# Optimization experiments

Hardware: AMD Instinct MI355X
Metric: run time of the kernel (lower is better)

The kernel has to match this reference:

```python
import jax, jax.numpy as jnp
import numpy as np

NEG_SLOPE = 0.2


def _gat_layer(x, W, a_src, a_dst, src, dst, ew, num_nodes):
    # Dense projection: [N, Din] @ [Din, Dout] -> [N, Dout]
    h = x @ W
    s = h @ a_src  # per-node source score, [N]
    d = h @ a_dst  # per-node destination score, [N]
    score = jax.nn.leaky_relu(s[src] + d[dst], NEG_SLOPE)  # [E]
    # segment softmax over incoming edges of each destination node
    m = jax.ops.segment_max(score, dst, num_segments=num_nodes)
    ex = jnp.exp(score - m[dst])
    denom = jax.ops.segment_sum(ex, dst, num_segments=num_nodes)
    alpha = ex / jnp.maximum(denom[dst], jnp.asarray(1e-16, ex.dtype))
    alpha = alpha * ew  # edge-weighted attention
    # gather h_j, scale by alpha, scatter-add into destinations
    return jax.ops.segment_sum(h[src] * alpha[:, None], dst, num_segments=num_nodes)


def setup_inputs() -> dict:
    key = jax.random.key(0)
    ks = jax.random.split(key, 9)
    N, E, F_IN, HID, NC = 100000, 1600000, 256, 64, 40
    x = jax.random.normal(ks[0], (N, F_IN), dtype=jnp.float32)
    edge_index = jax.random.randint(ks[1], (2, E), 0, N, dtype=jnp.int32)
    edge_weight = jax.random.uniform(ks[2], (E,), dtype=jnp.float32)
    W1 = jax.random.normal(ks[3], (F_IN, HID), dtype=jnp.float32) / np.sqrt(F_IN)
    a1_src = jax.random.normal(ks[4], (HID,), dtype=jnp.float32) / np.sqrt(HID)
    a1_dst = jax.random.normal(ks[5], (HID,), dtype=jnp.float32) / np.sqrt(HID)
    W2 = jax.random.normal(ks[6], (HID, NC), dtype=jnp.float32) / np.sqrt(HID)
    a2_src = jax.random.normal(ks[7], (NC,), dtype=jnp.float32) / np.sqrt(NC)
    a2_dst = jax.random.normal(ks[8], (NC,), dtype=jnp.float32) / np.sqrt(NC)
    return {"x": x, "edge_index": edge_index, "edge_weight": edge_weight,
            "W1": W1, "a1_src": a1_src, "a1_dst": a1_dst,
            "W2": W2, "a2_src": a2_src, "a2_dst": a2_dst}


def reference(x, edge_index, edge_weight, W1, a1_src, a1_dst, W2, a2_src, a2_dst):
    N = x.shape[0]
    # add_self_loops=True in both convs: append (i, i) edges with weight 1
    loops = jnp.arange(N, dtype=edge_index.dtype)
    src = jnp.concatenate([edge_index[0], loops])
    dst = jnp.concatenate([edge_index[1], loops])
    ew = jnp.concatenate([edge_weight, jnp.ones((N,), edge_weight.dtype)])
    h = jax.nn.relu(_gat_layer(x, W1, a1_src, a1_dst, src, dst, ew, N))
    # dropout inactive in eval mode
    out = _gat_layer(h, W2, a2_src, a2_dst, src, dst, ew, N)
    return out
```

## Files before the change

kernel.cpp:

```cpp
#include <hip/hip_runtime.h>
#include <hip/hip_bf16.h>
#include <math.h>

#define NEG_SLOPE 0.2f

typedef __attribute__((ext_vector_type(4))) float f32x4;
typedef __attribute__((ext_vector_type(8))) short bf16x8;
typedef __attribute__((ext_vector_type(4))) short bf16x4;

__device__ __forceinline__ float leaky(float x) { return x > 0.f ? x : NEG_SLOPE * x; }

__device__ __forceinline__ unsigned short bf_hi(float x) {
  return (unsigned short)(__float_as_uint(x) >> 16);
}

__device__ __forceinline__ unsigned short bf_rne(float x) {
  unsigned u = __float_as_uint(x);
  return (unsigned short)((u + 0x7FFFu + ((u >> 16) & 1u)) >> 16);
}


#define BIN_CHUNK 4096
#define BCAP 8192

__global__ void k_curinit(int* __restrict__ cursor, int NB) {
  int i = blockIdx.x * blockDim.x + threadIdx.x;
  if (i < NB) cursor[i] = i * BCAP;
}

__global__ __launch_bounds__(256)
void k_bin(const int* __restrict__ ei, const float* __restrict__ ew, int E, int N,
           int* __restrict__ cursor, int2* __restrict__ staged, int NB) {
  __shared__ int lhist[512];
  __shared__ int lbase[512];
  int tid = threadIdx.x;
  int start = blockIdx.x * BIN_CHUNK;
  int NT = E + N;
  int srcv[16], dstv[16]; float wv[16];
#pragma unroll
  for (int j = 0; j < 16; j++) {
    int e = start + j * 256 + tid;
    int s = 0, d = -1; float w = 0.f;
    if (e < NT) {
      if (e < E) { s = ei[e]; d = ei[E + e]; w = ew[e]; }
      else       { s = d = e - E; w = 1.f; }
    }
    srcv[j] = s; dstv[j] = d; wv[j] = w;
  }
  for (int b = tid; b < NB; b += 256) lhist[b] = 0;
  __syncthreads();
#pragma unroll
  for (int j = 0; j < 16; j++)
    if (dstv[j] >= 0) atomicAdd(&lhist[dstv[j] >> 8], 1);
  __syncthreads();
  for (int b = tid; b < NB; b += 256) {
    int n = lhist[b];
    lbase[b] = (n > 0) ? atomicAdd(&cursor[b], n) : 0;
    lhist[b] = 0;
  }
  __syncthreads();
#pragma unroll
  for (int j = 0; j < 16; j++) {
    if (dstv[j] >= 0) {
      int bkt = dstv[j] >> 8;
      int off = atomicAdd(&lhist[bkt], 1);
      staged[lbase[bkt] + off] =
          make_int2(srcv[j] | ((dstv[j] & 255) << 24), __float_as_int(wv[j]));
    }
  }
}

__global__ void k_bscan(const int* __restrict__ cursor, int NB, int NT, int N,
                        int* __restrict__ bbase, int* __restrict__ rp) {
  __shared__ int sm[1024];
  for (int j = threadIdx.x; j < NB; j += blockDim.x)
    sm[j] = cursor[j] - j * BCAP;
  __syncthreads();
  if (threadIdx.x == 0) {
    int run = 0;
    for (int j = 0; j < NB; j++) { int t = sm[j]; sm[j] = run; run += t; }
    sm[NB] = run;
  }
  __syncthreads();
  for (int j = threadIdx.x; j <= NB; j += blockDim.x) bbase[j] = sm[j];
  if (threadIdx.x == 0) rp[N] = NT;
}

__global__ __launch_bounds__(256)
void k_finalize(const int2* __restrict__ staged, const int* __restrict__ bbase,
                int N, int* __restrict__ rp, int2* __restrict__ csr) {
  __shared__ int cnt[256];
  __shared__ int sm[256];
  int b = blockIdx.x, tid = threadIdx.x;
  int sbase = b * BCAP;
  int cbase = bbase[b];
  int size = bbase[b + 1] - cbase;
  cnt[tid] = 0;
  __syncthreads();
  for (int i = tid; i < size; i += 256) {
    int2 v = staged[sbase + i];
    atomicAdd(&cnt[((unsigned)v.x) >> 24], 1);
  }
  __syncthreads();
  int s = cnt[tid];
  sm[tid] = s;
  __syncthreads();
  for (int off = 1; off < 256; off <<= 1) {
    int v = sm[tid];
    int add = (tid >= off) ? sm[tid - off] : 0;
    __syncthreads();
    sm[tid] = v + add;
    __syncthreads();
  }
  int excl = sm[tid] - s;
  int node = (b << 8) + tid;
  if (node < N) rp[node] = cbase + excl;
  cnt[tid] = excl;
  __syncthreads();
  for (int i = tid; i < size; i += 256) {
    int2 v = staged[sbase + i];
    int dlow = ((unsigned)v.x) >> 24;
    int pos = cbase + atomicAdd(&cnt[dlow], 1);
    csr[pos] = make_int2(v.x & 0x00FFFFFF, v.y);
  }
}

__global__ __launch_bounds__(256)
void k_wprep(const float* __restrict__ W, int K, int Mout,
             unsigned short* __restrict__ whi, unsigned short* __restrict__ wlo) {
  int idx = blockIdx.x * 256 + threadIdx.x;
  if (idx >= K * 64) return;
  int k = idx >> 6, n = idx & 63;
  float v = (n < Mout) ? W[(size_t)k * Mout + n] : 0.f;
  unsigned short h = bf_hi(v);
  float hf = __uint_as_float((unsigned)h << 16);
  unsigned short l = bf_hi(v - hf);
  int kc = k >> 5, kk = k & 31, quad = kk >> 3, j = kk & 7;
  int ct = n >> 4, nn = n & 15;
  int off = (((kc * 4 + ct) * 64) + quad * 16 + nn) * 8 + j;
  whi[off] = h; wlo[off] = l;
}

__global__ __launch_bounds__(256)
void k_gemm_mfma(const float* __restrict__ X, int K,
                 const unsigned short* __restrict__ WHI, const unsigned short* __restrict__ WLO,
                 const float* __restrict__ ASRC, const float* __restrict__ ADST, int Mout,
                 float* __restrict__ Hf, unsigned short* __restrict__ Hb, int ldH,
                 float* __restrict__ S, float* __restrict__ D, int N) {
  __shared__ __align__(16) unsigned short xhi[2048], xlo[2048];
  __shared__ __align__(16) unsigned short whs[2048], wls[2048];
  int tid = threadIdx.x;
  int lane = tid & 63, w = tid >> 6;
  int rowBase = blockIdx.x * 64;

  f32x4 acc[4];
#pragma unroll
  for (int c = 0; c < 4; c++) acc[c] = (f32x4){0.f, 0.f, 0.f, 0.f};

  int q0 = tid, q1 = tid + 256;
  int row0 = q0 >> 3, k40 = (q0 & 7) << 2;
  int row1 = q1 >> 3, k41 = (q1 & 7) << 2;
  int xo0 = (((row0 >> 4) * 64) + (k40 >> 3) * 16 + (row0 & 15)) * 8 + (k40 & 7);
  int xo1 = (((row1 >> 4) * 64) + (k41 >> 3) * 16 + (row1 & 15)) * 8 + (k41 & 7);
  int grow0 = rowBase + row0, grow1 = rowBase + row1;

  int nch = K >> 5;
  f32x4 xr0, xr1; bf16x8 wh, wl;

  xr0 = (f32x4){0.f, 0.f, 0.f, 0.f}; xr1 = xr0;
  if (grow0 < N) xr0 = *(const f32x4*)&X[(size_t)grow0 * K + k40];
  if (grow1 < N) xr1 = *(const f32x4*)&X[(size_t)grow1 * K + k41];
  wh = *(const bf16x8*)(WHI + tid * 8);
  wl = *(const bf16x8*)(WLO + tid * 8);

  for (int kc = 0; kc < nch; kc++) {
    bf16x4 h4, l4;
#pragma unroll
    for (int i = 0; i < 4; i++) {
      unsigned short h = bf_hi(xr0[i]);
      float hf = __uint_as_float((unsigned)h << 16);
      h4[i] = (short)h; l4[i] = (short)bf_hi(xr0[i] - hf);
    }
    *(bf16x4*)(xhi + xo0) = h4; *(bf16x4*)(xlo + xo0) = l4;
#pragma unroll
    for (int i = 0; i < 4; i++) {
      unsigned short h = bf_hi(xr1[i]);
      float hf = __uint_as_float((unsigned)h << 16);
      h4[i] = (short)h; l4[i] = (short)bf_hi(xr1[i] - hf);
    }
    *(bf16x4*)(xhi + xo1) = h4; *(bf16x4*)(xlo + xo1) = l4;
    *(bf16x8*)(whs + tid * 8) = wh;
    *(bf16x8*)(wls + tid * 8) = wl;
    __syncthreads();

    if (kc + 1 < nch) {
      int kb = (kc + 1) << 5;
      xr0 = (f32x4){0.f, 0.f, 0.f, 0.f}; xr1 = xr0;
      if (grow0 < N) xr0 = *(const f32x4*)&X[(size_t)grow0 * K + kb + k40];
      if (grow1 < N) xr1 = *(const f32x4*)&X[(size_t)grow1 * K + kb + k41];
      wh = *(const bf16x8*)(WHI + (size_t)(kc + 1) * 2048 + tid * 8);
      wl = *(const bf16x8*)(WLO + (size_t)(kc + 1) * 2048 + tid * 8);
    }

    bf16x8 ah = *(const bf16x8*)(xhi + (w * 64 + lane) * 8);
    bf16x8 al = *(const bf16x8*)(xlo + (w * 64 + lane) * 8);
#pragma unroll
    for (int c = 0; c < 4; c++) {
      bf16x8 bh = *(const bf16x8*)(whs + (c * 64 + lane) * 8);
      bf16x8 bl = *(const bf16x8*)(wls + (c * 64 + lane) * 8);
      acc[c] = __builtin_amdgcn_mfma_f32_16x16x32_bf16(ah, bh, acc[c], 0, 0, 0);
      acc[c] = __builtin_amdgcn_mfma_f32_16x16x32_bf16(ah, bl, acc[c], 0, 0, 0);
      acc[c] = __builtin_amdgcn_mfma_f32_16x16x32_bf16(al, bh, acc[c], 0, 0, 0);
    }
    __syncthreads();
  }

  int nn = lane & 15, quad = lane >> 4;
  float as_[4], ad_[4];
#pragma unroll
  for (int c = 0; c < 4; c++) {
    int col = c * 16 + nn;
    as_[c] = (col < Mout) ? ASRC[col] : 0.f;
    ad_[c] = (col < Mout) ? ADST[col] : 0.f;
  }
#pragma unroll
  for (int r = 0; r < 4; r++) {
    int grow = rowBase + w * 16 + quad * 4 + r;
    float ps = 0.f, pd = 0.f;
#pragma unroll
    for (int c = 0; c < 4; c++) {
      float v = acc[c][r];
      int col = c * 16 + nn;
      if (grow < N && col < Mout) {
        if (Hb) Hb[(size_t)grow * ldH + col] = bf_rne(v);
        else    Hf[(size_t)grow * ldH + col] = v;
      }
      ps += v * as_[c]; pd += v * ad_[c];
    }
#pragma unroll
    for (int off = 1; off < 16; off <<= 1) {
      ps += __shfl_xor(ps, off);
      pd += __shfl_xor(pd, off);
    }
    if (nn == 0 && grow < N) { S[grow] = ps; D[grow] = pd; }
  }
}

template <bool BF16>
__global__ __launch_bounds__(256)
void k_agg_fused(const int* __restrict__ rp, const int2* __restrict__ csr,
                 const float* __restrict__ S, const float* __restrict__ D,
                 const void* __restrict__ HinV, int ldh,
                 float* __restrict__ Out, int F4, int ldo, int do_relu, int N) {
  int gw = (blockIdx.x * blockDim.x + threadIdx.x) >> 6;
  int lane = threadIdx.x & 63;
  int sub = lane >> 4, fl = lane & 15;
  int node = gw * 4 + sub;
  bool active = node < N;
  bool fless = fl < F4;
  int b = 0, e = 1; float dd = 0.f;
  if (active) { b = rp[node]; e = rp[node + 1]; dd = D[node]; }
  float m = -1e30f, den = 0.f;
  f32x4 acc = (f32x4){0.f, 0.f, 0.f, 0.f};

  int need = e - b;
  need = max(need, __shfl_xor(need, 16));
  need = max(need, __shfl_xor(need, 32));
  int iters = (need + 3) >> 2;
  int last = e - 1;

  int t = b;
  for (int it = 0; it < iters; it++, t += 4) {
    int  idx[4]; float wgt[4], sv[4], cc[4], ex[4]; f32x4 hv[4];
#pragma unroll
    for (int j = 0; j < 4; j++) {
      int tj = t + j < e ? t + j : last;
      int2 p = csr[tj];
      idx[j] = p.x;
      wgt[j] = (t + j < e) ? __int_as_float(p.y) : 0.f;
    }
#pragma unroll
    for (int j = 0; j < 4; j++) sv[j] = S[idx[j]];
#pragma unroll
    for (int j = 0; j < 4; j++) {
      hv[j] = (f32x4){0.f, 0.f, 0.f, 0.f};
      if (fless) {
        if (BF16) {
          const unsigned short* Hb = (const unsigned short*)HinV;
          ushort4 uv = *(const ushort4*)(Hb + (size_t)idx[j] * ldh + (fl << 2));
          hv[j][0] = __uint_as_float((unsigned)uv.x << 16);
          hv[j][1] = __uint_as_float((unsigned)uv.y << 16);
          hv[j][2] = __uint_as_float((unsigned)uv.z << 16);
          hv[j][3] = __uint_as_float((unsigned)uv.w << 16);
        } else {
          const float* Hf = (const float*)HinV;
          hv[j] = *(const f32x4*)&Hf[(size_t)idx[j] * ldh + (fl << 2)];
        }
      }
    }
#pragma unroll
    for (int j = 0; j < 4; j++) cc[j] = (t + j < e) ? leaky(sv[j] + dd) : -1e30f;
    float bm = m;
#pragma unroll
    for (int j = 0; j < 4; j++) bm = fmaxf(bm, cc[j]);
    float r = __expf(m - bm);
    m = bm;
#pragma unroll
    for (int j = 0; j < 4; j++) ex[j] = (t + j < e) ? __expf(cc[j] - m) : 0.f;
    den = den * r + ((ex[0] + ex[1]) + (ex[2] + ex[3]));
    acc = acc * r + hv[0] * (ex[0] * wgt[0]) + hv[1] * (ex[1] * wgt[1])
                  + hv[2] * (ex[2] * wgt[2]) + hv[3] * (ex[3] * wgt[3]);
  }

  if (active && fless) {
    float inv = 1.0f / fmaxf(den, 1e-16f);
    f32x4 o = acc * inv;
    if (do_relu) {
#pragma unroll
      for (int j = 0; j < 4; j++) o[j] = fmaxf(o[j], 0.f);
    }
    *(f32x4*)&Out[(size_t)node * ldo + (fl << 2)] = o;
  }
}

extern "C" void kernel_launch(void* const* d_in, const int* in_sizes, int n_in,
                              void* d_out, int out_size, void* d_ws, size_t ws_size,
                              hipStream_t stream) {
  const float* x   = (const float*)d_in[0];
  const int*   ei  = (const int*)d_in[1];
  const float* ew  = (const float*)d_in[2];
  const float* W1  = (const float*)d_in[3];
  const float* a1s = (const float*)d_in[4];
  const float* a1d = (const float*)d_in[5];
  const float* W2  = (const float*)d_in[6];
  const float* a2s = (const float*)d_in[7];
  const float* a2d = (const float*)d_in[8];

  const int HID = in_sizes[4];
  const int NC  = in_sizes[7];
  const int FIN = in_sizes[3] / HID;
  const int N   = in_sizes[0] / FIN;
  const int E   = in_sizes[2];
  const int NT  = E + N;
  const int NB  = (N + 255) >> 8;
  float* out = (float*)d_out;

  char* wsb = (char*)d_ws;
  size_t off = 0;
  auto alloc = [&](size_t bytes) -> char* {
    char* p = wsb + off;
    off += (bytes + 255) & ~(size_t)255;
    return p;
  };
  unsigned short* h1b = (unsigned short*)alloc((size_t)N * 64 * 2);
  float* h2     = (float*)alloc((size_t)N * 64 * 4);
  float* g2     = (float*)alloc((size_t)N * 40 * 4);
  float* S      = (float*)alloc((size_t)N * 4);
  float* D      = (float*)alloc((size_t)N * 4);
  int*   rp     = (int*)alloc((size_t)(N + 1) * 4);
  int*   bbase  = (int*)alloc((size_t)(NB + 1) * 4);
  int*   cursor = (int*)alloc((size_t)NB * 4);
  int2*  csr    = (int2*)alloc((size_t)NT * 8);
  int2*  staged = (int2*)alloc((size_t)NB * BCAP * 8);
  unsigned short* whi1 = (unsigned short*)alloc((size_t)FIN * 64 * 2);
  unsigned short* wlo1 = (unsigned short*)alloc((size_t)FIN * 64 * 2);
  unsigned short* whi2 = (unsigned short*)alloc((size_t)HID * 64 * 2);
  unsigned short* wlo2 = (unsigned short*)alloc((size_t)HID * 64 * 2);
  (void)ws_size; (void)n_in; (void)out_size;

  const int ebins = (NT + BIN_CHUNK - 1) / BIN_CHUNK;

  hipLaunchKernelGGL(k_curinit, dim3((NB + 255) / 256), dim3(256), 0, stream, cursor, NB);
  hipLaunchKernelGGL(k_bin, dim3(ebins), dim3(256), 0, stream, ei, ew, E, N, cursor, staged, NB);
  hipLaunchKernelGGL(k_bscan, dim3(1), dim3(256), 0, stream, cursor, NB, NT, N, bbase, rp);
  hipLaunchKernelGGL(k_finalize, dim3(NB), dim3(256), 0, stream, staged, bbase, N, rp, csr);

  hipLaunchKernelGGL(k_wprep, dim3((FIN * 64 + 255) / 256), dim3(256), 0, stream,
                     W1, FIN, HID, whi1, wlo1);
  hipLaunchKernelGGL(k_wprep, dim3((HID * 64 + 255) / 256), dim3(256), 0, stream,
                     W2, HID, NC, whi2, wlo2);

  const int gblocks = (N + 63) / 64;
  const int ablocks = (N + 15) / 16;

  hipLaunchKernelGGL(k_gemm_mfma, dim3(gblocks), dim3(256), 0, stream,
                     x, FIN, whi1, wlo1, a1s, a1d, HID, (float*)nullptr, h1b, 64, S, D, N);
  hipLaunchKernelGGL((k_agg_fused<true>), dim3(ablocks), dim3(256), 0, stream,
                     rp, csr, S, D, (const void*)h1b, 64, h2, 16, 64, 1, N);

  hipLaunchKernelGGL(k_gemm_mfma, dim3(gblocks), dim3(256), 0, stream,
                     h2, HID, whi2, wlo2, a2s, a2d, NC, g2, (unsigned short*)nullptr, 40, S, D, N);
  hipLaunchKernelGGL((k_agg_fused<false>), dim3(ablocks), dim3(256), 0, stream,
                     rp, csr, S, D, (const void*)g2, 40, out, 10, NC, 0, N);
}
```

Baseline: 358.0 us.

## Precompute softmax edge coefficients in separate pass, simplify aggregation loop

```diff
diff --git a/kernel.cpp b/kernel.cpp
--- a/kernel.cpp
+++ b/kernel.cpp
@@ -20,7 +20,7 @@
 }
 
 
-#define BIN_CHUNK 4096
+#define BIN_CHUNK 2048
 #define BCAP 8192
 
 __global__ void k_curinit(int* __restrict__ cursor, int NB) {
@@ -36,9 +36,9 @@
   int tid = threadIdx.x;
   int start = blockIdx.x * BIN_CHUNK;
   int NT = E + N;
-  int srcv[16], dstv[16]; float wv[16];
-#pragma unroll
-  for (int j = 0; j < 16; j++) {
+  int srcv[8], dstv[8]; float wv[8];
+#pragma unroll
+  for (int j = 0; j < 8; j++) {
     int e = start + j * 256 + tid;
     int s = 0, d = -1; float w = 0.f;
     if (e < NT) {
@@ -50,7 +50,7 @@
   for (int b = tid; b < NB; b += 256) lhist[b] = 0;
   __syncthreads();
 #pragma unroll
-  for (int j = 0; j < 16; j++)
+  for (int j = 0; j < 8; j++)
     if (dstv[j] >= 0) atomicAdd(&lhist[dstv[j] >> 8], 1);
   __syncthreads();
   for (int b = tid; b < NB; b += 256) {
@@ -60,7 +60,7 @@
   }
   __syncthreads();
 #pragma unroll
-  for (int j = 0; j < 16; j++) {
+  for (int j = 0; j < 8; j++) {
     if (dstv[j] >= 0) {
       int bkt = dstv[j] >> 8;
       int off = atomicAdd(&lhist[bkt], 1);
@@ -70,23 +70,26 @@
   }
 }
 
-__global__ void k_bscan(const int* __restrict__ cursor, int NB, int NT, int N,
-                        int* __restrict__ bbase, int* __restrict__ rp) {
-  __shared__ int sm[1024];
-  for (int j = threadIdx.x; j < NB; j += blockDim.x)
-    sm[j] = cursor[j] - j * BCAP;
-  __syncthreads();
-  if (threadIdx.x == 0) {
-    int run = 0;
-    for (int j = 0; j < NB; j++) { int t = sm[j]; sm[j] = run; run += t; }
-    sm[NB] = run;
-  }
-  __syncthreads();
-  for (int j = threadIdx.x; j <= NB; j += blockDim.x) bbase[j] = sm[j];
-  if (threadIdx.x == 0) rp[N] = NT;
-}
-
-__global__ __launch_bounds__(256)
+__global__ __launch_bounds__(512)
+void k_bscan(const int* __restrict__ cursor, int NB, int NT, int N,
+             int* __restrict__ bbase, int* __restrict__ rp) {
+  __shared__ int sm[512];
+  int tid = threadIdx.x;
+  int v = (tid < NB) ? cursor[tid] - tid * BCAP : 0;
+  sm[tid] = v;
+  __syncthreads();
+  for (int off = 1; off < 512; off <<= 1) {
+    int x = sm[tid];
+    int a = (tid >= off) ? sm[tid - off] : 0;
+    __syncthreads();
+    sm[tid] = x + a;
+    __syncthreads();
+  }
+  if (tid < NB) bbase[tid] = sm[tid] - v;
+  if (tid == 0) { bbase[NB] = sm[NB - 1]; rp[N] = NT; }
+}
+
+__global__ __launch_bounds__(512)
 void k_finalize(const int2* __restrict__ staged, const int* __restrict__ bbase,
                 int N, int* __restrict__ rp, int2* __restrict__ csr) {
   __shared__ int cnt[256];
@@ -95,29 +98,31 @@
   int sbase = b * BCAP;
   int cbase = bbase[b];
   int size = bbase[b + 1] - cbase;
-  cnt[tid] = 0;
-  __syncthreads();
-  for (int i = tid; i < size; i += 256) {
+  if (tid < 256) cnt[tid] = 0;
+  __syncthreads();
+  for (int i = tid; i < size; i += 512) {
     int2 v = staged[sbase + i];
     atomicAdd(&cnt[((unsigned)v.x) >> 24], 1);
   }
   __syncthreads();
-  int s = cnt[tid];
-  sm[tid] = s;
+  int s = 0;
+  if (tid < 256) { s = cnt[tid]; sm[tid] = s; }
   __syncthreads();
   for (int off = 1; off < 256; off <<= 1) {
-    int v = sm[tid];
-    int add = (tid >= off) ? sm[tid - off] : 0;
-    __syncthreads();
-    sm[tid] = v + add;
-    __syncthreads();
-  }
-  int excl = sm[tid] - s;
-  int node = (b << 8) + tid;
-  if (node < N) rp[node] = cbase + excl;
-  cnt[tid] = excl;
-  __syncthreads();
-  for (int i = tid; i < size; i += 256) {
+    int x = 0;
+    if (tid < 256) { x = sm[tid]; if (tid >= off) x += sm[tid - off]; }
+    __syncthreads();
+    if (tid < 256) sm[tid] = x;
+    __syncthreads();
+  }
+  if (tid < 256) {
+    int excl = sm[tid] - s;
+    int node = (b << 8) + tid;
+    if (node < N) rp[node] = cbase + excl;
+    cnt[tid] = excl;
+  }
+  __syncthreads();
+  for (int i = tid; i < size; i += 512) {
     int2 v = staged[sbase + i];
     int dlow = ((unsigned)v.x) >> 24;
     int pos = cbase + atomicAdd(&cnt[dlow], 1);
@@ -246,10 +251,52 @@
   }
 }
 
+__global__ __launch_bounds__(256)
+void k_coef(const int* __restrict__ rp, const int2* __restrict__ csr,
+            const float* __restrict__ S, const float* __restrict__ D,
+            int2* __restrict__ ec, int N) {
+  int gw = (blockIdx.x * blockDim.x + threadIdx.x) >> 6;
+  int lane = threadIdx.x & 63;
+  int sub = lane >> 4, fl = lane & 15;
+  int node = gw * 4 + sub;
+  int b = 0, e = 0; float dd = 0.f;
+  if (node < N) { b = rp[node]; e = rp[node + 1]; dd = D[node]; }
+  float m = -1e30f, den = 0.f;
+  for (int t = b; t < e; t += 16) {
+    int i = t + fl;
+    bool v = i < e;
+    int2 p = csr[v ? i : e - 1];
+    float c = v ? leaky(S[p.x] + dd) : -1e30f;
+    float bm = c;
+    bm = fmaxf(bm, __shfl_xor(bm, 1));
+    bm = fmaxf(bm, __shfl_xor(bm, 2));
+    bm = fmaxf(bm, __shfl_xor(bm, 4));
+    bm = fmaxf(bm, __shfl_xor(bm, 8));
+    bm = fmaxf(bm, m);
+    float r = __expf(m - bm);
+    float ex = v ? __expf(c - bm) : 0.f;
+    ex += __shfl_xor(ex, 1);
+    ex += __shfl_xor(ex, 2);
+    ex += __shfl_xor(ex, 4);
+    ex += __shfl_xor(ex, 8);
+    den = den * r + ex;
+    m = bm;
+  }
+  float inv = 1.f / fmaxf(den, 1e-16f);
+  for (int t = b; t < e; t += 16) {
+    int i = t + fl;
+    if (i < e) {
+      int2 p = csr[i];
+      float c = leaky(S[p.x] + dd);
+      float coef = __expf(c - m) * __int_as_float(p.y) * inv;
+      ec[i] = make_int2(p.x, __float_as_int(coef));
+    }
+  }
+}
+
 template <bool BF16>
 __global__ __launch_bounds__(256)
-void k_agg_fused(const int* __restrict__ rp, const int2* __restrict__ csr,
-                 const float* __restrict__ S, const float* __restrict__ D,
+void k_agg_fused(const int* __restrict__ rp, const int2* __restrict__ ec,
                  const void* __restrict__ HinV, int ldh,
                  float* __restrict__ Out, int F4, int ldo, int do_relu, int N) {
   int gw = (blockIdx.x * blockDim.x + threadIdx.x) >> 6;
@@ -258,31 +305,29 @@
   int node = gw * 4 + sub;
   bool active = node < N;
   bool fless = fl < F4;
-  int b = 0, e = 1; float dd = 0.f;
-  if (active) { b = rp[node]; e = rp[node + 1]; dd = D[node]; }
-  float m = -1e30f, den = 0.f;
-  f32x4 acc = (f32x4){0.f, 0.f, 0.f, 0.f};
+  int b = 0, e = 1;
+  if (active) { b = rp[node]; e = rp[node + 1]; }
+  f32x4 acc0 = (f32x4){0.f, 0.f, 0.f, 0.f};
+  f32x4 acc1 = (f32x4){0.f, 0.f, 0.f, 0.f};
 
   int need = e - b;
   need = max(need, __shfl_xor(need, 16));
   need = max(need, __shfl_xor(need, 32));
-  int iters = (need + 3) >> 2;
+  int iters = (need + 7) >> 3;
   int last = e - 1;
 
   int t = b;
-  for (int it = 0; it < iters; it++, t += 4) {
-    int  idx[4]; float wgt[4], sv[4], cc[4], ex[4]; f32x4 hv[4];
-#pragma unroll
-    for (int j = 0; j < 4; j++) {
+  for (int it = 0; it < iters; it++, t += 8) {
+    int idx[8]; float cf[8]; f32x4 hv[8];
+#pragma unroll
+    for (int j = 0; j < 8; j++) {
       int tj = t + j < e ? t + j : last;
-      int2 p = csr[tj];
+      int2 p = ec[tj];
       idx[j] = p.x;
-      wgt[j] = (t + j < e) ? __int_as_float(p.y) : 0.f;
-    }
-#pragma unroll
-    for (int j = 0; j < 4; j++) sv[j] = S[idx[j]];
-#pragma unroll
-    for (int j = 0; j < 4; j++) {
+      cf[j] = (t + j < e) ? __int_as_float(p.y) : 0.f;
+    }
+#pragma unroll
+    for (int j = 0; j < 8; j++) {
       hv[j] = (f32x4){0.f, 0.f, 0.f, 0.f};
       if (fless) {
         if (BF16) {
@@ -299,22 +344,14 @@
       }
     }
 #pragma unroll
-    for (int j = 0; j < 4; j++) cc[j] = (t + j < e) ? leaky(sv[j] + dd) : -1e30f;
-    float bm = m;
-#pragma unroll
-    for (int j = 0; j < 4; j++) bm = fmaxf(bm, cc[j]);
-    float r = __expf(m - bm);
-    m = bm;
-#pragma unroll
-    for (int j = 0; j < 4; j++) ex[j] = (t + j < e) ? __expf(cc[j] - m) : 0.f;
-    den = den * r + ((ex[0] + ex[1]) + (ex[2] + ex[3]));
-    acc = acc * r + hv[0] * (ex[0] * wgt[0]) + hv[1] * (ex[1] * wgt[1])
-                  + hv[2] * (ex[2] * wgt[2]) + hv[3] * (ex[3] * wgt[3]);
+    for (int j = 0; j < 8; j += 2) {
+      acc0 += hv[j] * cf[j];
+      acc1 += hv[j + 1] * cf[j + 1];
+    }
   }
 
   if (active && fless) {
-    float inv = 1.0f / fmaxf(den, 1e-16f);
-    f32x4 o = acc * inv;
+    f32x4 o = acc0 + acc1;
     if (do_relu) {
 #pragma unroll
       for (int j = 0; j < 4; j++) o[j] = fmaxf(o[j], 0.f);
@@ -366,14 +403,15 @@
   unsigned short* wlo1 = (unsigned short*)alloc((size_t)FIN * 64 * 2);
   unsigned short* whi2 = (unsigned short*)alloc((size_t)HID * 64 * 2);
   unsigned short* wlo2 = (unsigned short*)alloc((size_t)HID * 64 * 2);
+  int2* ec = staged;
   (void)ws_size; (void)n_in; (void)out_size;
 
   const int ebins = (NT + BIN_CHUNK - 1) / BIN_CHUNK;
 
   hipLaunchKernelGGL(k_curinit, dim3((NB + 255) / 256), dim3(256), 0, stream, cursor, NB);
   hipLaunchKernelGGL(k_bin, dim3(ebins), dim3(256), 0, stream, ei, ew, E, N, cursor, staged, NB);
-  hipLaunchKernelGGL(k_bscan, dim3(1), dim3(256), 0, stream, cursor, NB, NT, N, bbase, rp);
-  hipLaunchKernelGGL(k_finalize, dim3(NB), dim3(256), 0, stream, staged, bbase, N, rp, csr);
+  hipLaunchKernelGGL(k_bscan, dim3(1), dim3(512), 0, stream, cursor, NB, NT, N, bbase, rp);
+  hipLaunchKernelGGL(k_finalize, dim3(NB), dim3(512), 0, stream, staged, bbase, N, rp, csr);
 
   hipLaunchKernelGGL(k_wprep, dim3((FIN * 64 + 255) / 256), dim3(256), 0, stream,
                      W1, FIN, HID, whi1, wlo1);
@@ -385,11 +423,13 @@
 
   hipLaunchKernelGGL(k_gemm_mfma, dim3(gblocks), dim3(256), 0, stream,
                      x, FIN, whi1, wlo1, a1s, a1d, HID, (float*)nullptr, h1b, 64, S, D, N);
+  hipLaunchKernelGGL(k_coef, dim3(ablocks), dim3(256), 0, stream, rp, csr, S, D, ec, N);
   hipLaunchKernelGGL((k_agg_fused<true>), dim3(ablocks), dim3(256), 0, stream,
-                     rp, csr, S, D, (const void*)h1b, 64, h2, 16, 64, 1, N);
+                     rp, ec, (const void*)h1b, 64, h2, 16, 64, 1, N);
 
   hipLaunchKernelGGL(k_gemm_mfma, dim3(gblocks), dim3(256), 0, stream,
                      h2, HID, whi2, wlo2, a2s, a2d, NC, g2, (unsigned short*)nullptr, 40, S, D, N);
+  hipLaunchKernelGGL(k_coef, dim3(ablocks), dim3(256), 0, stream, rp, csr, S, D, ec, N);
   hipLaunchKernelGGL((k_agg_fused<false>), dim3(ablocks), dim3(256), 0, stream,
-                     rp, csr, S, D, (const void*)g2, 40, out, 10, NC, 0, N);
-}
+                     rp, ec, (const void*)g2, 40, out, 10, NC, 0, N);
+}
```

After: 402.9 us. 1.13x slower.
